# Kernel tuning notes

Measured on AMD Instinct MI355X. Metric: run time of the kernel, lower is better.

Reference implementation:

```python
import jax, jax.numpy as jnp
import numpy as np

N_NODES = 100000
N_EDGES = 1600000
IN_CH = 128
HID = 128
OUT = 128


def gcn_conv(x, src, dst, dinv, W, b, n_nodes):
    """GCNConv with self-loops already folded into (src, dst, dinv).
    out[v] = sum_{(u->v)} dinv[u]*dinv[v] * (x @ W)[u] + b
    """
    xw = x @ W                                   # [N, F_out]
    norm = dinv[src] * dinv[dst]                 # [E+N]
    msg = xw[src] * norm[:, None]                # [E+N, F_out] (gather)
    out = jax.ops.segment_sum(msg, dst, num_segments=n_nodes)  # scatter-add
    return out + b


def setup_inputs() -> dict:
    key = jax.random.key(0)
    k = jax.random.split(key, 8)
    x = jax.random.normal(k[0], (N_NODES, IN_CH), dtype=jnp.float32)
    edge_index = jax.random.randint(k[1], (2, N_EDGES), 0, N_NODES, dtype=jnp.int64)
    s = 0.05
    W1 = jax.random.normal(k[2], (IN_CH, HID), dtype=jnp.float32) * s
    b1 = jnp.zeros((HID,), dtype=jnp.float32)
    W2 = jax.random.normal(k[3], (HID, HID), dtype=jnp.float32) * s
    b2 = jnp.zeros((HID,), dtype=jnp.float32)
    Wfc = jax.random.normal(k[4], (HID, OUT), dtype=jnp.float32) * s
    bfc = jnp.zeros((OUT,), dtype=jnp.float32)
    return {"x": x, "edge_index": edge_index, "W1": W1, "b1": b1,
            "W2": W2, "b2": b2, "Wfc": Wfc, "bfc": bfc}


def reference(x, edge_index, W1, b1, W2, b2, Wfc, bfc):
    n = x.shape[0]
    loop = jnp.arange(n, dtype=edge_index.dtype)
    src = jnp.concatenate([edge_index[0], loop])   # add self loops (PyG default)
    dst = jnp.concatenate([edge_index[1], loop])
    # symmetric normalization: deg over targets incl. self loops
    deg = jax.ops.segment_sum(jnp.ones_like(dst, dtype=x.dtype), dst, num_segments=n)
    dinv = jnp.where(deg > 0, jax.lax.rsqrt(deg), 0.0)
    h = jax.nn.relu(gcn_conv(x, src, dst, dinv, W1, b1, n))
    h = jax.nn.relu(gcn_conv(h, src, dst, dinv, W2, b2, n))
    pooled = jnp.mean(h, axis=0, keepdims=True)    # [1, HID]
    return pooled @ Wfc + bfc                      # [1, OUT]
```

## Files before the change

### kernel.cpp

```cpp
#include <hip/hip_runtime.h>
#include <stdint.h>

typedef unsigned short ushort_t;
typedef __attribute__((ext_vector_type(8))) short bf16x8;
typedef __attribute__((ext_vector_type(4))) float f32x4;
typedef __attribute__((ext_vector_type(2))) float f32x2;

#define BKT_SHIFT 7
#define BKT_W     128
#define NB_MAX    1024
#define KB_THREADS 1024
#define KB_EPT    4
#define KB_CHUNK  (KB_THREADS * KB_EPT)
#define BCAP      2560
#define CSTRIDE   2944
#define CSR_THREADS 512
#define PSLICES   1024


__device__ __forceinline__ ushort_t f2bf(float f) {
    union { float f; uint32_t u; } a; a.f = f;
    uint32_t u = a.u;
    uint32_t r = (u + 0x7FFFu + ((u >> 16) & 1u)) >> 16;
    return (ushort_t)r;
}
__device__ __forceinline__ float bf_lo(uint32_t p) { return __uint_as_float(p << 16); }
__device__ __forceinline__ float bf_hi(uint32_t p) { return __uint_as_float(p & 0xFFFF0000u); }

__global__ __launch_bounds__(256) void kW_init(const float* __restrict__ W1,
                                               const float* __restrict__ W2,
                                               ushort_t* __restrict__ Wt1,
                                               ushort_t* __restrict__ Wt2,
                                               int* __restrict__ bcnt,
                                               float* __restrict__ pooled,
                                               uint8_t* __restrict__ xwq, int n) {
    int b = blockIdx.x, t = threadIdx.x;
    if (b < 64) {
        int i = b * 256 + t;
        int k = i >> 7, nn = i & 127;
        Wt1[nn * 128 + k] = f2bf(W1[i]);
        Wt2[nn * 128 + k] = f2bf(W2[i]);
    } else {
        const int tid = (b - 64) * 256 + t;
        const int zs = 16 * 256;
        for (int i = tid; i < PSLICES * 128; i += zs) pooled[i] = 0.f;
        for (int i = tid; i < NB_MAX; i += zs) bcnt[i] = 0;
        if (tid < 32) ((uint32_t*)(xwq + (size_t)n * 128))[tid] = 0u;
    }
}

__global__ __launch_bounds__(KB_THREADS) void kB_bucket(const int* __restrict__ src,
                                                        const int* __restrict__ dst, int E, int NB,
                                                        int* __restrict__ bcnt,
                                                        uint32_t* __restrict__ bpack) {
    __shared__ int lh[NB_MAX];
    const int t = threadIdx.x;
    for (int i = t; i < NB; i += KB_THREADS) lh[i] = 0;
    __syncthreads();

    const int base = blockIdx.x * KB_CHUNK + t * KB_EPT;
    int d[KB_EPT], rank[KB_EPT];
    const bool full = (base + KB_EPT - 1 < E);
    if (full) {
        int4 dv = *(const int4*)(dst + base);
        d[0] = dv.x; d[1] = dv.y; d[2] = dv.z; d[3] = dv.w;
#pragma unroll
        for (int i = 0; i < KB_EPT; i++)
            rank[i] = atomicAdd(&lh[d[i] >> BKT_SHIFT], 1);
    } else {
#pragma unroll
        for (int i = 0; i < KB_EPT; i++) {
            int e = base + i;
            if (e < E) {
                d[i] = dst[e];
                rank[i] = atomicAdd(&lh[d[i] >> BKT_SHIFT], 1);
            } else {
                d[i] = -1; rank[i] = 0;
            }
        }
    }
    __syncthreads();
    for (int i = t; i < NB; i += KB_THREADS) {
        int c = lh[i];
        lh[i] = c ? atomicAdd(&bcnt[i], c) : 0;
    }
    __syncthreads();
    if (full) {
        int4 sv = *(const int4*)(src + base);
        int s[KB_EPT] = {sv.x, sv.y, sv.z, sv.w};
#pragma unroll
        for (int i = 0; i < KB_EPT; i++) {
            int bkt = d[i] >> BKT_SHIFT;
            size_t pos = (size_t)bkt * BCAP + lh[bkt] + rank[i];
            bpack[pos] = ((uint32_t)s[i] << BKT_SHIFT) | (uint32_t)(d[i] & (BKT_W - 1));
        }
    } else {
#pragma unroll
        for (int i = 0; i < KB_EPT; i++) {
            if (d[i] >= 0) {
                int bkt = d[i] >> BKT_SHIFT;
                size_t pos = (size_t)bkt * BCAP + lh[bkt] + rank[i];
                bpack[pos] = ((uint32_t)src[base + i] << BKT_SHIFT) | (uint32_t)(d[i] & (BKT_W - 1));
            }
        }
    }
}

__global__ __launch_bounds__(CSR_THREADS) void kC_csr(const uint32_t* __restrict__ bpack,
                                                      const int* __restrict__ bcnt, int NB, int n,
                                                      float* __restrict__ dinv,
                                                      int* __restrict__ offs,
                                                      int* __restrict__ ends,
                                                      int* __restrict__ csr) {
    __shared__ int pr[BKT_W];
    __shared__ int cnt[BKT_W];
    __shared__ int cur[BKT_W];
    __shared__ int pend[BKT_W];

    const int t = threadIdx.x;
    const int b = blockIdx.x;
    const int nb0 = b << BKT_SHIFT;
    const int wlen = min(BKT_W, n - nb0);
    const int cntb = bcnt[b];
    const uint32_t* bp = bpack + (size_t)b * BCAP;
    const int base = b * CSTRIDE;

    if (t < BKT_W) cnt[t] = 0;
    __syncthreads();
    for (int e = t; e < cntb; e += CSR_THREADS)
        atomicAdd(&cnt[bp[e] & (BKT_W - 1)], 1);
    __syncthreads();

    int v = (t < BKT_W) ? cnt[t] : 0;
    int pv = (v + 3) & ~3;
    if (t < BKT_W) pr[t] = pv;
    __syncthreads();
    for (int off = 1; off < BKT_W; off <<= 1) {
        int x = (t >= off && t < BKT_W) ? pr[t - off] : 0;
        __syncthreads();
        if (t < BKT_W) pr[t] += x;
        __syncthreads();
    }
    if (t < BKT_W) {
        int st = base + pr[t] - pv;
        cur[t] = st;
        pend[t] = st + pv;
        if (t < wlen) {
            offs[nb0 + t] = st;
            ends[nb0 + t] = st + pv;
            dinv[nb0 + t] = rsqrtf((float)(v + 1));
        }
    }
    __syncthreads();

    for (int e = t; e < cntb; e += CSR_THREADS) {
        uint32_t p = bp[e];
        int pos = atomicAdd(&cur[p & (BKT_W - 1)], 1);
        csr[pos] = (int)(p >> BKT_SHIFT);
    }
    __syncthreads();
    if (t < BKT_W) {
        int qe = pend[t];
        for (int q = cur[t]; q < qe; q++) csr[q] = n;
    }
}

__global__ __launch_bounds__(256) void k_gemm1(const float* __restrict__ x,
                                               const ushort_t* __restrict__ Wt,
                                               const float* __restrict__ dinv,
                                               uint8_t* __restrict__ C, int n) {
    __shared__ ushort_t al[64 * 136];
    __shared__ ushort_t wl[128 * 136];
    const int t = threadIdx.x;
    const int l = t & 63;
    const int wave = t >> 6;
    const int lane15 = l & 15;
    const int quad = l >> 4;
    const int m0 = blockIdx.x * 64;
    const int rows = min(64, n - m0);

#pragma unroll
    for (int i = 0; i < 8; i++) {
        int f = t + 256 * i;
        int r = f >> 4, c = f & 15;
        *(uint4*)(&wl[r * 136 + c * 8]) = ((const uint4*)Wt)[f];
    }
    {
        const float4* Ap = (const float4*)(x + (size_t)m0 * 128);
        int nf = rows * 32;
#pragma unroll
        for (int i = 0; i < 8; i++) {
            int f = t + 256 * i;
            float4 vv = make_float4(0.f, 0.f, 0.f, 0.f);
            if (f < nf) vv = Ap[f];
            ushort4 us;
            us.x = f2bf(vv.x); us.y = f2bf(vv.y); us.z = f2bf(vv.z); us.w = f2bf(vv.w);
            int r = f >> 5, c = f & 31;
            *(ushort4*)(&al[r * 136 + c * 4]) = us;
        }
    }
    __syncthreads();

    f32x4 acc[8];
#pragma unroll
    for (int nt = 0; nt < 8; nt++) acc[nt] = (f32x4){0.f, 0.f, 0.f, 0.f};

    const int arow = wave * 16 + lane15;
#pragma unroll
    for (int kt = 0; kt < 4; kt++) {
        bf16x8 af = *(const bf16x8*)(&al[arow * 136 + kt * 32 + quad * 8]);
#pragma unroll
        for (int nt = 0; nt < 8; nt++) {
            bf16x8 bfr = *(const bf16x8*)(&wl[(nt * 16 + lane15) * 136 + kt * 32 + quad * 8]);
            acc[nt] = __builtin_amdgcn_mfma_f32_16x16x32_bf16(af, bfr, acc[nt], 0, 0, 0);
        }
    }

    const int rbase = m0 + wave * 16 + quad * 4;
    float dsc[4];
#pragma unroll
    for (int r = 0; r < 4; r++)
        dsc[r] = (rbase + r < n) ? dinv[rbase + r] : 0.f;
#pragma unroll
    for (int nt = 0; nt < 8; nt++) {
        int c0 = nt * 16 + lane15;
#pragma unroll
        for (int r = 0; r < 4; r += 2) {
            int pk = __builtin_amdgcn_cvt_pk_fp8_f32(acc[nt][r] * dsc[r],
                                                     acc[nt][r + 1] * dsc[r + 1], 0, false);
            int row0 = rbase + r, row1 = rbase + r + 1;
            if (row0 < n) C[(size_t)row0 * 128 + c0] = (uint8_t)pk;
            if (row1 < n) C[(size_t)row1 * 128 + c0] = (uint8_t)(pk >> 8);
        }
    }
}

__global__ __launch_bounds__(256) void k_gemm_mfma(const ushort_t* __restrict__ A,
                                                   const ushort_t* __restrict__ Wt,
                                                   const float* __restrict__ dinv,
                                                   uint8_t* __restrict__ C, int n) {
    __shared__ ushort_t al[64 * 136];
    __shared__ ushort_t wl[128 * 136];
    const int t = threadIdx.x;
    const int l = t & 63;
    const int wave = t >> 6;
    const int lane15 = l & 15;
    const int quad = l >> 4;
    const int m0 = blockIdx.x * 64;
    const int rows = min(64, n - m0);

#pragma unroll
    for (int i = 0; i < 8; i++) {
        int f = t + 256 * i;
        int r = f >> 4, c = f & 15;
        *(uint4*)(&wl[r * 136 + c * 8]) = ((const uint4*)Wt)[f];
    }
    {
        const uint4* Ap = (const uint4*)(A + (size_t)m0 * 128);
        int nf = rows * 16;
#pragma unroll
        for (int i = 0; i < 4; i++) {
            int f = t + 256 * i;
            uint4 v = make_uint4(0, 0, 0, 0);
            if (f < nf) v = Ap[f];
            int r = f >> 4, c = f & 15;
            *(uint4*)(&al[r * 136 + c * 8]) = v;
        }
    }
    __syncthreads();

    f32x4 acc[8];
#pragma unroll
    for (int nt = 0; nt < 8; nt++) acc[nt] = (f32x4){0.f, 0.f, 0.f, 0.f};

    const int arow = wave * 16 + lane15;
#pragma unroll
    for (int kt = 0; kt < 4; kt++) {
        bf16x8 af = *(const bf16x8*)(&al[arow * 136 + kt * 32 + quad * 8]);
#pragma unroll
        for (int nt = 0; nt < 8; nt++) {
            bf16x8 bfr = *(const bf16x8*)(&wl[(nt * 16 + lane15) * 136 + kt * 32 + quad * 8]);
            acc[nt] = __builtin_amdgcn_mfma_f32_16x16x32_bf16(af, bfr, acc[nt], 0, 0, 0);
        }
    }

    const int rbase = m0 + wave * 16 + quad * 4;
    float dsc[4];
#pragma unroll
    for (int r = 0; r < 4; r++)
        dsc[r] = (rbase + r < n) ? dinv[rbase + r] : 0.f;
#pragma unroll
    for (int nt = 0; nt < 8; nt++) {
        int c0 = nt * 16 + lane15;
#pragma unroll
        for (int r = 0; r < 4; r += 2) {
            int pk = __builtin_amdgcn_cvt_pk_fp8_f32(acc[nt][r] * dsc[r],
                                                     acc[nt][r + 1] * dsc[r + 1], 0, false);
            int row0 = rbase + r, row1 = rbase + r + 1;
            if (row0 < n) C[(size_t)row0 * 128 + c0] = (uint8_t)pk;
            if (row1 < n) C[(size_t)row1 * 128 + c0] = (uint8_t)(pk >> 8);
        }
    }
}

__global__ __launch_bounds__(256) void k_agg(const ushort_t* __restrict__ xw,
                                             const int* __restrict__ offsets,
                                             const int* __restrict__ ends,
                                             const int* __restrict__ csr,
                                             const float* __restrict__ dinv,
                                             const float* __restrict__ bias,
                                             ushort_t* __restrict__ out, int n,
                                             float* __restrict__ pooled) {
    __shared__ float red[512];
    const int l = threadIdx.x & 63;
    const int wave = (blockIdx.x << 2) | (threadIdx.x >> 6);
    const int wstride = gridDim.x << 2;
    const float2 bb = ((const float2*)bias)[l];
    uint32_t* out32 = (uint32_t*)out;
    float psx = 0.f, psy = 0.f;

    for (int v = wave; v < n; v += wstride) {
        uint32_t pv = (uint32_t)xw[(size_t)v * 64 + l];
        f32x2 fs = __builtin_amdgcn_cvt_pk_f32_fp8((int)pv, false);
        float ax = fs.x, ay = fs.y;

        int e  = __builtin_amdgcn_readfirstlane(offsets[v]);
        int e1 = __builtin_amdgcn_readfirstlane(ends[v]);

        for (; e + 15 < e1; e += 16) {
            const int4* c4 = (const int4*)(csr + e);
            int4 w0 = c4[0], w1 = c4[1], w2 = c4[2], w3 = c4[3];
            int u[16];
            u[0]  = __builtin_amdgcn_readfirstlane(w0.x);
            u[1]  = __builtin_amdgcn_readfirstlane(w0.y);
            u[2]  = __builtin_amdgcn_readfirstlane(w0.z);
            u[3]  = __builtin_amdgcn_readfirstlane(w0.w);
            u[4]  = __builtin_amdgcn_readfirstlane(w1.x);
            u[5]  = __builtin_amdgcn_readfirstlane(w1.y);
            u[6]  = __builtin_amdgcn_readfirstlane(w1.z);
            u[7]  = __builtin_amdgcn_readfirstlane(w1.w);
            u[8]  = __builtin_amdgcn_readfirstlane(w2.x);
            u[9]  = __builtin_amdgcn_readfirstlane(w2.y);
            u[10] = __builtin_amdgcn_readfirstlane(w2.z);
            u[11] = __builtin_amdgcn_readfirstlane(w2.w);
            u[12] = __builtin_amdgcn_readfirstlane(w3.x);
            u[13] = __builtin_amdgcn_readfirstlane(w3.y);
            u[14] = __builtin_amdgcn_readfirstlane(w3.z);
            u[15] = __builtin_amdgcn_readfirstlane(w3.w);
            uint32_t p[16];
#pragma unroll
            for (int i = 0; i < 16; i++) p[i] = (uint32_t)xw[(size_t)u[i] * 64 + l];
#pragma unroll
            for (int i = 0; i < 16; i++) {
                f32x2 f = __builtin_amdgcn_cvt_pk_f32_fp8((int)p[i], false);
                ax += f.x; ay += f.y;
            }
        }
        for (; e + 7 < e1; e += 8) {
            const int4* c4 = (const int4*)(csr + e);
            int4 w0 = c4[0], w1 = c4[1];
            int u[8];
            u[0] = __builtin_amdgcn_readfirstlane(w0.x);
            u[1] = __builtin_amdgcn_readfirstlane(w0.y);
            u[2] = __builtin_amdgcn_readfirstlane(w0.z);
            u[3] = __builtin_amdgcn_readfirstlane(w0.w);
            u[4] = __builtin_amdgcn_readfirstlane(w1.x);
            u[5] = __builtin_amdgcn_readfirstlane(w1.y);
            u[6] = __builtin_amdgcn_readfirstlane(w1.z);
            u[7] = __builtin_amdgcn_readfirstlane(w1.w);
            uint32_t p[8];
#pragma unroll
            for (int i = 0; i < 8; i++) p[i] = (uint32_t)xw[(size_t)u[i] * 64 + l];
#pragma unroll
            for (int i = 0; i < 8; i++) {
                f32x2 f = __builtin_amdgcn_cvt_pk_f32_fp8((int)p[i], false);
                ax += f.x; ay += f.y;
            }
        }
        for (; e + 3 < e1; e += 4) {
            int4 w0 = *(const int4*)(csr + e);
            int u[4];
            u[0] = __builtin_amdgcn_readfirstlane(w0.x);
            u[1] = __builtin_amdgcn_readfirstlane(w0.y);
            u[2] = __builtin_amdgcn_readfirstlane(w0.z);
            u[3] = __builtin_amdgcn_readfirstlane(w0.w);
            uint32_t p[4];
#pragma unroll
            for (int i = 0; i < 4; i++) p[i] = (uint32_t)xw[(size_t)u[i] * 64 + l];
#pragma unroll
            for (int i = 0; i < 4; i++) {
                f32x2 f = __builtin_amdgcn_cvt_pk_f32_fp8((int)p[i], false);
                ax += f.x; ay += f.y;
            }
        }

        float dv = dinv[v];
        float ox = fmaxf(fmaf(ax, dv, bb.x), 0.f);
        float oy = fmaxf(fmaf(ay, dv, bb.y), 0.f);
        if (pooled == nullptr) {
            out32[(size_t)v * 64 + l] = ((uint32_t)f2bf(oy) << 16) | (uint32_t)f2bf(ox);
        } else {
            psx += ox; psy += oy;
        }
    }

    if (pooled != nullptr) {
        const int t = threadIdx.x;
        red[t] = psx;
        red[256 + t] = psy;
        __syncthreads();
        if (t < 64) {
            float sx = red[t] + red[t + 64] + red[t + 128] + red[t + 192];
            float sy = red[256 + t] + red[256 + t + 64] + red[256 + t + 128] + red[256 + t + 192];
            float* slice = pooled + (size_t)(blockIdx.x & (PSLICES - 1)) * 128;
            atomicAdd(&slice[2 * t], sx);
            atomicAdd(&slice[2 * t + 1], sy);
        }
    }
}

__global__ __launch_bounds__(512) void k_fc(const float* __restrict__ pooled,
                                            const float* __restrict__ Wfc,
                                            const float* __restrict__ bfc,
                                            float* __restrict__ out, float invN) {
    __shared__ f32x4 red4[512];
    __shared__ float pl[128];
    __shared__ float wf[128 * 128];
    const int t = threadIdx.x;
    const int q = t & 31;
    const int g = t >> 5;

    const f32x4* W4 = (const f32x4*)Wfc;
    f32x4* wf4 = (f32x4*)wf;
#pragma unroll
    for (int i = 0; i < 8; i++) wf4[t + 512 * i] = W4[t + 512 * i];

    const f32x4* P = (const f32x4*)pooled;
    f32x4 a0 = (f32x4){0.f, 0.f, 0.f, 0.f}, a1 = a0, a2 = a0, a3 = a0;
#pragma unroll
    for (int k = 0; k < 16; k++) {
        a0 += P[(size_t)(g + 16 * (4 * k + 0)) * 32 + q];
        a1 += P[(size_t)(g + 16 * (4 * k + 1)) * 32 + q];
        a2 += P[(size_t)(g + 16 * (4 * k + 2)) * 32 + q];
        a3 += P[(size_t)(g + 16 * (4 * k + 3)) * 32 + q];
    }
    red4[t] = (a0 + a1) + (a2 + a3);
    __syncthreads();
    if (t < 32) {
        f32x4 s = red4[t];
#pragma unroll
        for (int g2 = 1; g2 < 16; g2++) s += red4[g2 * 32 + t];
        pl[4 * t + 0] = s[0] * invN;
        pl[4 * t + 1] = s[1] * invN;
        pl[4 * t + 2] = s[2] * invN;
        pl[4 * t + 3] = s[3] * invN;
    }
    __syncthreads();
    if (t < 128) {
        float o = bfc[t];
#pragma unroll 8
        for (int k = 0; k < 128; k++) o = fmaf(pl[k], wf[k * 128 + t], o);
        out[t] = o;
    }
}

extern "C" void kernel_launch(void* const* d_in, const int* in_sizes, int n_in,
                              void* d_out, int out_size, void* d_ws, size_t ws_size,
                              hipStream_t stream) {
    const float* x    = (const float*)d_in[0];
    const int*   ei   = (const int*)d_in[1];
    const float* W1   = (const float*)d_in[2];
    const float* b1   = (const float*)d_in[3];
    const float* W2   = (const float*)d_in[4];
    const float* b2   = (const float*)d_in[5];
    const float* Wfc  = (const float*)d_in[6];
    const float* bfc  = (const float*)d_in[7];
    float*       out  = (float*)d_out;

    const int n = in_sizes[0] / 128;
    const int E = in_sizes[1] / 2;
    const int* src = ei;
    const int* dst = ei + E;
    const int NB = (n + BKT_W - 1) >> BKT_SHIFT;

    char* w = (char*)d_ws;
    uint8_t*  xwq = (uint8_t*)w;  w += (size_t)(n + 1) * 128;
    ushort_t* h   = (ushort_t*)w; w += (size_t)n * 128 * sizeof(ushort_t);
    int*      csr = (int*)w;      w += (size_t)NB * CSTRIDE * sizeof(int);
    uint32_t* bpack = (uint32_t*)w; w += (size_t)NB * BCAP * sizeof(uint32_t);
    float* dinv = (float*)w;  w += (size_t)n * sizeof(float);
    int*   offs = (int*)w;    w += (size_t)n * sizeof(int);
    int*   ends = (int*)w;    w += (size_t)n * sizeof(int);
    w = (char*)(((uintptr_t)w + 127) & ~(uintptr_t)127);
    int*   bcnt  = (int*)w;   w += NB_MAX * sizeof(int);
    float* pooled = (float*)w; w += (size_t)PSLICES * 128 * sizeof(float);
    ushort_t* Wt1 = (ushort_t*)w; w += 16384 * sizeof(ushort_t);
    ushort_t* Wt2 = (ushort_t*)w; w += 16384 * sizeof(ushort_t);

    const int ntiles64 = (n + 63) / 64;
    const float invN = 1.0f / (float)n;

    kW_init<<<80, 256, 0, stream>>>(W1, W2, Wt1, Wt2, bcnt, pooled, xwq, n);
    kB_bucket<<<(E + KB_CHUNK - 1) / KB_CHUNK, KB_THREADS, 0, stream>>>(src, dst, E, NB, bcnt, bpack);
    kC_csr<<<NB, CSR_THREADS, 0, stream>>>(bpack, bcnt, NB, n, dinv, offs, ends, csr);
    k_gemm1<<<ntiles64, 256, 0, stream>>>(x, Wt1, dinv, xwq, n);

    k_agg<<<8192, 256, 0, stream>>>((const ushort_t*)xwq, offs, ends, csr, dinv, b1, h, n, nullptr);
    k_gemm_mfma<<<ntiles64, 256, 0, stream>>>(h, Wt2, dinv, xwq, n);
    k_agg<<<8192, 256, 0, stream>>>((const ushort_t*)xwq, offs, ends, csr, dinv, b2, h, n, pooled);

    k_fc<<<1, 512, 0, stream>>>(pooled, Wfc, bfc, out, invN);
}
```

Before: 240.4 us.

## Process four contiguous nodes per wave with prefetched CSR heads and interleaved offsets

Each wave in the aggregation kernel now handles four consecutive nodes instead of grid-striding. It loads their start/end pairs from a new interleaved offset array with two vector loads, and prefetches the next node's first CSR indices so the first gathers are issued early. The goal is to hide the dependent-load latency chain of offsets, then indices, then feature gathers. In exchange it needs extra padding in the csr and offset buffers and adds register pressure. It also relies on the grid covering all nodes with no stride loop.

```diff
diff --git a/kernel.cpp b/kernel.cpp
--- a/kernel.cpp
+++ b/kernel.cpp
@@ -33,7 +33,8 @@
                                                ushort_t* __restrict__ Wt2,
                                                int* __restrict__ bcnt,
                                                float* __restrict__ pooled,
-                                               uint8_t* __restrict__ xwq, int n) {
+                                               uint8_t* __restrict__ xwq,
+                                               int* __restrict__ oe, int n) {
     int b = blockIdx.x, t = threadIdx.x;
     if (b < 64) {
         int i = b * 256 + t;
@@ -46,6 +47,7 @@
         for (int i = tid; i < PSLICES * 128; i += zs) pooled[i] = 0.f;
         for (int i = tid; i < NB_MAX; i += zs) bcnt[i] = 0;
         if (tid < 32) ((uint32_t*)(xwq + (size_t)n * 128))[tid] = 0u;
+        if (tid < 16) oe[2 * n + tid] = 0;
     }
 }
 
@@ -109,8 +111,7 @@
 __global__ __launch_bounds__(CSR_THREADS) void kC_csr(const uint32_t* __restrict__ bpack,
                                                       const int* __restrict__ bcnt, int NB, int n,
                                                       float* __restrict__ dinv,
-                                                      int* __restrict__ offs,
-                                                      int* __restrict__ ends,
+                                                      int* __restrict__ oe,
                                                       int* __restrict__ csr) {
     __shared__ int pr[BKT_W];
     __shared__ int cnt[BKT_W];
@@ -146,8 +147,7 @@
         cur[t] = st;
         pend[t] = st + pv;
         if (t < wlen) {
-            offs[nb0 + t] = st;
-            ends[nb0 + t] = st + pv;
+            *(int2*)(oe + 2 * (nb0 + t)) = make_int2(st, st + pv);
             dinv[nb0 + t] = rsqrtf((float)(v + 1));
         }
     }
@@ -304,8 +304,7 @@
 }
 
 __global__ __launch_bounds__(256) void k_agg(const ushort_t* __restrict__ xw,
-                                             const int* __restrict__ offsets,
-                                             const int* __restrict__ ends,
+                                             const int* __restrict__ oe,
                                              const int* __restrict__ csr,
                                              const float* __restrict__ dinv,
                                              const float* __restrict__ bias,
@@ -313,94 +312,145 @@
                                              float* __restrict__ pooled) {
     __shared__ float red[512];
     const int l = threadIdx.x & 63;
-    const int wave = (blockIdx.x << 2) | (threadIdx.x >> 6);
-    const int wstride = gridDim.x << 2;
+    const int wid = (blockIdx.x << 2) | (threadIdx.x >> 6);
+    const int v0 = wid << 2;
     const float2 bb = ((const float2*)bias)[l];
     uint32_t* out32 = (uint32_t*)out;
     float psx = 0.f, psy = 0.f;
 
-    for (int v = wave; v < n; v += wstride) {
-        uint32_t pv = (uint32_t)xw[(size_t)v * 64 + l];
-        f32x2 fs = __builtin_amdgcn_cvt_pk_f32_fp8((int)pv, false);
-        float ax = fs.x, ay = fs.y;
-
-        int e  = __builtin_amdgcn_readfirstlane(offsets[v]);
-        int e1 = __builtin_amdgcn_readfirstlane(ends[v]);
-
-        for (; e + 15 < e1; e += 16) {
-            const int4* c4 = (const int4*)(csr + e);
-            int4 w0 = c4[0], w1 = c4[1], w2 = c4[2], w3 = c4[3];
-            int u[16];
-            u[0]  = __builtin_amdgcn_readfirstlane(w0.x);
-            u[1]  = __builtin_amdgcn_readfirstlane(w0.y);
-            u[2]  = __builtin_amdgcn_readfirstlane(w0.z);
-            u[3]  = __builtin_amdgcn_readfirstlane(w0.w);
-            u[4]  = __builtin_amdgcn_readfirstlane(w1.x);
-            u[5]  = __builtin_amdgcn_readfirstlane(w1.y);
-            u[6]  = __builtin_amdgcn_readfirstlane(w1.z);
-            u[7]  = __builtin_amdgcn_readfirstlane(w1.w);
-            u[8]  = __builtin_amdgcn_readfirstlane(w2.x);
-            u[9]  = __builtin_amdgcn_readfirstlane(w2.y);
-            u[10] = __builtin_amdgcn_readfirstlane(w2.z);
-            u[11] = __builtin_amdgcn_readfirstlane(w2.w);
-            u[12] = __builtin_amdgcn_readfirstlane(w3.x);
-            u[13] = __builtin_amdgcn_readfirstlane(w3.y);
-            u[14] = __builtin_amdgcn_readfirstlane(w3.z);
-            u[15] = __builtin_amdgcn_readfirstlane(w3.w);
-            uint32_t p[16];
-#pragma unroll
-            for (int i = 0; i < 16; i++) p[i] = (uint32_t)xw[(size_t)u[i] * 64 + l];
-#pragma unroll
-            for (int i = 0; i < 16; i++) {
-                f32x2 f = __builtin_amdgcn_cvt_pk_f32_fp8((int)p[i], false);
-                ax += f.x; ay += f.y;
-            }
-        }
-        for (; e + 7 < e1; e += 8) {
-            const int4* c4 = (const int4*)(csr + e);
-            int4 w0 = c4[0], w1 = c4[1];
-            int u[8];
-            u[0] = __builtin_amdgcn_readfirstlane(w0.x);
-            u[1] = __builtin_amdgcn_readfirstlane(w0.y);
-            u[2] = __builtin_amdgcn_readfirstlane(w0.z);
-            u[3] = __builtin_amdgcn_readfirstlane(w0.w);
-            u[4] = __builtin_amdgcn_readfirstlane(w1.x);
-            u[5] = __builtin_amdgcn_readfirstlane(w1.y);
-            u[6] = __builtin_amdgcn_readfirstlane(w1.z);
-            u[7] = __builtin_amdgcn_readfirstlane(w1.w);
-            uint32_t p[8];
-#pragma unroll
-            for (int i = 0; i < 8; i++) p[i] = (uint32_t)xw[(size_t)u[i] * 64 + l];
-#pragma unroll
-            for (int i = 0; i < 8; i++) {
-                f32x2 f = __builtin_amdgcn_cvt_pk_f32_fp8((int)p[i], false);
-                ax += f.x; ay += f.y;
-            }
-        }
-        for (; e + 3 < e1; e += 4) {
-            int4 w0 = *(const int4*)(csr + e);
-            int u[4];
-            u[0] = __builtin_amdgcn_readfirstlane(w0.x);
-            u[1] = __builtin_amdgcn_readfirstlane(w0.y);
-            u[2] = __builtin_amdgcn_readfirstlane(w0.z);
-            u[3] = __builtin_amdgcn_readfirstlane(w0.w);
-            uint32_t p[4];
-#pragma unroll
-            for (int i = 0; i < 4; i++) p[i] = (uint32_t)xw[(size_t)u[i] * 64 + l];
-#pragma unroll
-            for (int i = 0; i < 4; i++) {
-                f32x2 f = __builtin_amdgcn_cvt_pk_f32_fp8((int)p[i], false);
-                ax += f.x; ay += f.y;
-            }
-        }
-
-        float dv = dinv[v];
-        float ox = fmaxf(fmaf(ax, dv, bb.x), 0.f);
-        float oy = fmaxf(fmaf(ay, dv, bb.y), 0.f);
-        if (pooled == nullptr) {
-            out32[(size_t)v * 64 + l] = ((uint32_t)f2bf(oy) << 16) | (uint32_t)f2bf(ox);
-        } else {
-            psx += ox; psy += oy;
+    if (v0 < n) {
+        const int nv = min(4, n - v0);
+        const int4* oh = (const int4*)(oe + 2 * v0);
+        int4 h0 = oh[0], h1 = oh[1];
+        int e_[4], e1_[4];
+        e_[0]  = __builtin_amdgcn_readfirstlane(h0.x);
+        e1_[0] = __builtin_amdgcn_readfirstlane(h0.y);
+        e_[1]  = __builtin_amdgcn_readfirstlane(h0.z);
+        e1_[1] = __builtin_amdgcn_readfirstlane(h0.w);
+        e_[2]  = __builtin_amdgcn_readfirstlane(h1.x);
+        e1_[2] = __builtin_amdgcn_readfirstlane(h1.y);
+        e_[3]  = __builtin_amdgcn_readfirstlane(h1.z);
+        e1_[3] = __builtin_amdgcn_readfirstlane(h1.w);
+
+        uint32_t sv[4];
+#pragma unroll
+        for (int j = 0; j < 4; j++)
+            sv[j] = (j < nv) ? (uint32_t)xw[(size_t)(v0 + j) * 64 + l] : 0u;
+
+        int4 pf = *(const int4*)(csr + e_[0]);
+
+#pragma unroll
+        for (int j = 0; j < 4; j++) {
+            if (j >= nv) break;
+            const int v = v0 + j;
+            int e = e_[j];
+            const int e1 = e1_[j];
+            int4 pfn;
+            if (j < 3) pfn = *(const int4*)(csr + e_[j + 1]);
+
+            f32x2 fs = __builtin_amdgcn_cvt_pk_f32_fp8((int)sv[j], false);
+            float ax = fs.x, ay = fs.y;
+
+            uint32_t g0 = 0, g1 = 0, g2 = 0, g3 = 0;
+            const bool havepf = (e < e1);
+            if (havepf) {
+                int u0 = __builtin_amdgcn_readfirstlane(pf.x);
+                int u1 = __builtin_amdgcn_readfirstlane(pf.y);
+                int u2 = __builtin_amdgcn_readfirstlane(pf.z);
+                int u3 = __builtin_amdgcn_readfirstlane(pf.w);
+                g0 = (uint32_t)xw[(size_t)u0 * 64 + l];
+                g1 = (uint32_t)xw[(size_t)u1 * 64 + l];
+                g2 = (uint32_t)xw[(size_t)u2 * 64 + l];
+                g3 = (uint32_t)xw[(size_t)u3 * 64 + l];
+                e += 4;
+            }
+
+            for (; e + 15 < e1; e += 16) {
+                const int4* c4 = (const int4*)(csr + e);
+                int4 w0 = c4[0], w1 = c4[1], w2 = c4[2], w3 = c4[3];
+                int u[16];
+                u[0]  = __builtin_amdgcn_readfirstlane(w0.x);
+                u[1]  = __builtin_amdgcn_readfirstlane(w0.y);
+                u[2]  = __builtin_amdgcn_readfirstlane(w0.z);
+                u[3]  = __builtin_amdgcn_readfirstlane(w0.w);
+                u[4]  = __builtin_amdgcn_readfirstlane(w1.x);
+                u[5]  = __builtin_amdgcn_readfirstlane(w1.y);
+                u[6]  = __builtin_amdgcn_readfirstlane(w1.z);
+                u[7]  = __builtin_amdgcn_readfirstlane(w1.w);
+                u[8]  = __builtin_amdgcn_readfirstlane(w2.x);
+                u[9]  = __builtin_amdgcn_readfirstlane(w2.y);
+                u[10] = __builtin_amdgcn_readfirstlane(w2.z);
+                u[11] = __builtin_amdgcn_readfirstlane(w2.w);
+                u[12] = __builtin_amdgcn_readfirstlane(w3.x);
+                u[13] = __builtin_amdgcn_readfirstlane(w3.y);
+                u[14] = __builtin_amdgcn_readfirstlane(w3.z);
+                u[15] = __builtin_amdgcn_readfirstlane(w3.w);
+                uint32_t p[16];
+#pragma unroll
+                for (int i = 0; i < 16; i++) p[i] = (uint32_t)xw[(size_t)u[i] * 64 + l];
+#pragma unroll
+                for (int i = 0; i < 16; i++) {
+                    f32x2 f = __builtin_amdgcn_cvt_pk_f32_fp8((int)p[i], false);
+                    ax += f.x; ay += f.y;
+                }
+            }
+            for (; e + 7 < e1; e += 8) {
+                const int4* c4 = (const int4*)(csr + e);
+                int4 w0 = c4[0], w1 = c4[1];
+                int u[8];
+                u[0] = __builtin_amdgcn_readfirstlane(w0.x);
+                u[1] = __builtin_amdgcn_readfirstlane(w0.y);
+                u[2] = __builtin_amdgcn_readfirstlane(w0.z);
+                u[3] = __builtin_amdgcn_readfirstlane(w0.w);
+                u[4] = __builtin_amdgcn_readfirstlane(w1.x);
+                u[5] = __builtin_amdgcn_readfirstlane(w1.y);
+                u[6] = __builtin_amdgcn_readfirstlane(w1.z);
+                u[7] = __builtin_amdgcn_readfirstlane(w1.w);
+                uint32_t p[8];
+#pragma unroll
+                for (int i = 0; i < 8; i++) p[i] = (uint32_t)xw[(size_t)u[i] * 64 + l];
+#pragma unroll
+                for (int i = 0; i < 8; i++) {
+                    f32x2 f = __builtin_amdgcn_cvt_pk_f32_fp8((int)p[i], false);
+                    ax += f.x; ay += f.y;
+                }
+            }
+            for (; e + 3 < e1; e += 4) {
+                int4 w0 = *(const int4*)(csr + e);
+                int u0 = __builtin_amdgcn_readfirstlane(w0.x);
+                int u1 = __builtin_amdgcn_readfirstlane(w0.y);
+                int u2 = __builtin_amdgcn_readfirstlane(w0.z);
+                int u3 = __builtin_amdgcn_readfirstlane(w0.w);
+                uint32_t p0 = (uint32_t)xw[(size_t)u0 * 64 + l];
+                uint32_t p1 = (uint32_t)xw[(size_t)u1 * 64 + l];
+                uint32_t p2 = (uint32_t)xw[(size_t)u2 * 64 + l];
+                uint32_t p3 = (uint32_t)xw[(size_t)u3 * 64 + l];
+                f32x2 f0 = __builtin_amdgcn_cvt_pk_f32_fp8((int)p0, false);
+                f32x2 f1 = __builtin_amdgcn_cvt_pk_f32_fp8((int)p1, false);
+                f32x2 f2 = __builtin_amdgcn_cvt_pk_f32_fp8((int)p2, false);
+                f32x2 f3 = __builtin_amdgcn_cvt_pk_f32_fp8((int)p3, false);
+                ax += f0.x + f1.x + f2.x + f3.x;
+                ay += f0.y + f1.y + f2.y + f3.y;
+            }
+
+            if (havepf) {
+                f32x2 f0 = __builtin_amdgcn_cvt_pk_f32_fp8((int)g0, false);
+                f32x2 f1 = __builtin_amdgcn_cvt_pk_f32_fp8((int)g1, false);
+                f32x2 f2 = __builtin_amdgcn_cvt_pk_f32_fp8((int)g2, false);
+                f32x2 f3 = __builtin_amdgcn_cvt_pk_f32_fp8((int)g3, false);
+                ax += f0.x + f1.x + f2.x + f3.x;
+                ay += f0.y + f1.y + f2.y + f3.y;
+            }
+
+            float dv = dinv[v];
+            float ox = fmaxf(fmaf(ax, dv, bb.x), 0.f);
+            float oy = fmaxf(fmaf(ay, dv, bb.y), 0.f);
+            if (pooled == nullptr) {
+                out32[(size_t)v * 64 + l] = ((uint32_t)f2bf(oy) << 16) | (uint32_t)f2bf(ox);
+            } else {
+                psx += ox; psy += oy;
+            }
+            pf = pfn;
         }
     }
 
@@ -486,11 +536,10 @@
     char* w = (char*)d_ws;
     uint8_t*  xwq = (uint8_t*)w;  w += (size_t)(n + 1) * 128;
     ushort_t* h   = (ushort_t*)w; w += (size_t)n * 128 * sizeof(ushort_t);
-    int*      csr = (int*)w;      w += (size_t)NB * CSTRIDE * sizeof(int);
+    int*      csr = (int*)w;      w += ((size_t)NB * CSTRIDE + 64) * sizeof(int);
     uint32_t* bpack = (uint32_t*)w; w += (size_t)NB * BCAP * sizeof(uint32_t);
     float* dinv = (float*)w;  w += (size_t)n * sizeof(float);
-    int*   offs = (int*)w;    w += (size_t)n * sizeof(int);
-    int*   ends = (int*)w;    w += (size_t)n * sizeof(int);
+    int*   oe   = (int*)w;    w += (size_t)2 * (n + 8) * sizeof(int);
     w = (char*)(((uintptr_t)w + 127) & ~(uintptr_t)127);
     int*   bcnt  = (int*)w;   w += NB_MAX * sizeof(int);
     float* pooled = (float*)w; w += (size_t)PSLICES * 128 * sizeof(float);
@@ -500,14 +549,14 @@
     const int ntiles64 = (n + 63) / 64;
     const float invN = 1.0f / (float)n;
 
-    kW_init<<<80, 256, 0, stream>>>(W1, W2, Wt1, Wt2, bcnt, pooled, xwq, n);
+    kW_init<<<80, 256, 0, stream>>>(W1, W2, Wt1, Wt2, bcnt, pooled, xwq, oe, n);
     kB_bucket<<<(E + KB_CHUNK - 1) / KB_CHUNK, KB_THREADS, 0, stream>>>(src, dst, E, NB, bcnt, bpack);
-    kC_csr<<<NB, CSR_THREADS, 0, stream>>>(bpack, bcnt, NB, n, dinv, offs, ends, csr);
+    kC_csr<<<NB, CSR_THREADS, 0, stream>>>(bpack, bcnt, NB, n, dinv, oe, csr);
     k_gemm1<<<ntiles64, 256, 0, stream>>>(x, Wt1, dinv, xwq, n);
 
-    k_agg<<<8192, 256, 0, stream>>>((const ushort_t*)xwq, offs, ends, csr, dinv, b1, h, n, nullptr);
+    k_agg<<<8192, 256, 0, stream>>>((const ushort_t*)xwq, oe, csr, dinv, b1, h, n, nullptr);
     k_gemm_mfma<<<ntiles64, 256, 0, stream>>>(h, Wt2, dinv, xwq, n);
-    k_agg<<<8192, 256, 0, stream>>>((const ushort_t*)xwq, offs, ends, csr, dinv, b2, h, n, pooled);
+    k_agg<<<8192, 256, 0, stream>>>((const ushort_t*)xwq, oe, csr, dinv, b2, h, n, pooled);
 
     k_fc<<<1, 512, 0, stream>>>(pooled, Wfc, bfc, out, invN);
 }
```

New measurement: 239.3 us. No clear change (-0.5%).
